# Kernel optimization log

Hardware: AMD Instinct MI355X
Metric: run time of the kernel (lower is better)

The kernel has to match this reference:

```python
import jax, jax.numpy as jnp
import numpy as np

N = 512
BATCH = 128
EPS = 1e-08


def setup_inputs() -> dict:
    key = jax.random.key(0)
    kx, kb = jax.random.split(key)
    # binary indicator of which items are present in each set
    x = jax.random.randint(kx, (BATCH, N), 0, 2, dtype=jnp.int32)
    # column-normalized random feature matrix, as in the torch __init__
    B = jax.random.normal(kb, (N, N), dtype=jnp.float32)
    B = B / jnp.linalg.norm(B, axis=0, keepdims=True)
    return {"x": x, "B": B}


def reference(x, B):
    n = B.shape[0]
    I = jnp.eye(n, dtype=B.dtype)
    L = B.T @ B + EPS * I                      # (n, n) PSD kernel
    m = (x != 0).astype(B.dtype)               # (batch, n) active-item mask
    # zero out rows and cols of inactive items, put 1 on their diagonal
    Lb = L[None, :, :] * m[:, :, None] * m[:, None, :]   # (batch, n, n)
    Lb = Lb + I[None, :, :] * (1.0 - m)[:, None, :]
    _, logdet_b = jnp.linalg.slogdet(Lb)       # (batch,)
    _, logdet_Z = jnp.linalg.slogdet(L + I)    # scalar normalizer
    return logdet_b - logdet_Z
```

## Files before the change

kernel.cpp:

```cpp
#include <hip/hip_runtime.h>
#include <math.h>

#define N 512
#define BATCH 128
#define EPS 1e-8f
#define TPB 1024
#define NW 16
#define KP 304
#define LN2 0.69314718055994530942f
#define SPLIT 160
#define GSTR 160
#define SLD2 356
#define SLAB_BYTES (352 * SLD2 * 4)

typedef _Float16 f16;
typedef _Float16 f16x8 __attribute__((ext_vector_type(8)));
typedef float f32x4 __attribute__((ext_vector_type(4)));

__device__ __forceinline__ int lh_base(int r) {
    const int a = r >> 3, b = r & 7;
    return 8 * (a + 1) * (4 * a + b);
}

#define G1_OFF   26880
#define SCR0_OFF 94848
#define M0_OFF   113280
#define SCR1_OFF 139520
#define M1_OFF   157952
#define SCR2_OFF 126720
#define M2_OFF   145152
#define ARENA_SZ 160512

__device__ __forceinline__ float rdl(float v, int l) {
    return __builtin_bit_cast(float,
        __builtin_amdgcn_readlane(__builtin_bit_cast(int, v), l));
}

__device__ __forceinline__ void tri_map(int e, int* r_out, int* c_out) {
    int rr = (int)((sqrtf(8.0f * (float)e + 1.0f) - 1.0f) * 0.5f);
    while ((((rr + 1) * (rr + 2)) >> 1) <= e) ++rr;
    while (((rr * (rr + 1)) >> 1) > e) --rr;
    *r_out = rr;
    *c_out = e - ((rr * (rr + 1)) >> 1);
}

__global__ __launch_bounds__(256) void compute_L(const float* __restrict__ B,
                                                 float* __restrict__ L) {
    const int r0 = blockIdx.x * 64, c0 = blockIdx.y * 64;
    const int tx = threadIdx.x & 15, ty = threadIdx.x >> 4;
    __shared__ float Bi[16][64];
    __shared__ float Bj[16][64];
    float acc[4][4] = {};
    for (int k0 = 0; k0 < N; k0 += 16) {
#pragma unroll
        for (int q = 0; q < 4; ++q) {
            const int e = threadIdx.x + q * 256;
            const int kr = e >> 6, cc = e & 63;
            Bi[kr][cc] = B[(k0 + kr) * N + r0 + cc];
            Bj[kr][cc] = B[(k0 + kr) * N + c0 + cc];
        }
        __syncthreads();
#pragma unroll
        for (int kq = 0; kq < 16; ++kq) {
            float a[4], b[4];
#pragma unroll
            for (int q = 0; q < 4; ++q) {
                a[q] = Bi[kq][ty * 4 + q];
                b[q] = Bj[kq][tx * 4 + q];
            }
#pragma unroll
            for (int i = 0; i < 4; ++i)
#pragma unroll
                for (int j = 0; j < 4; ++j) acc[i][j] = fmaf(a[i], b[j], acc[i][j]);
        }
        __syncthreads();
    }
#pragma unroll
    for (int i = 0; i < 4; ++i) {
        const int r = r0 + ty * 4 + i;
        f32x4 v;
#pragma unroll
        for (int j = 0; j < 4; ++j) {
            const int c = c0 + tx * 4 + j;
            v[j] = acc[i][j] + ((r == c) ? EPS : 0.0f);
        }
        *(f32x4*)(&L[r * N + c0 + tx * 4]) = v;
    }
}

template <int MODE>
__device__ __forceinline__ float gath(const float* __restrict__ L,
                                      const float* __restrict__ S, const short* idx,
                                      int k, bool add1, int gr, int gc) {
    if constexpr (MODE <= 1) {
        if (gr < k && gc < k) {
            float v = L[(int)idx[gr] * N + (int)idx[gc]];
            if (add1 && gr == gc) v += 1.0f;
            return v;
        }
        return (gr == gc) ? 1.0f : 0.0f;
    } else {
        if (gr < k && gc < k) {
            const int r2 = gr > gc ? gr : gc, c2 = gr > gc ? gc : gr;
            return S[r2 * SLD2 + c2];
        }
        return (gr == gc) ? 1.0f : 0.0f;
    }
}

template <int MODE>
__device__ float chol32(char* arena, const float* __restrict__ S,
                        const float* __restrict__ L, const short* idx,
                        int k, int rows, int ncols, bool add1) {
    const int tid = threadIdx.x;
    const int lane = tid & 63, wv = tid >> 6;
    constexpr int scr_off = (MODE == 0) ? SCR0_OFF : (MODE == 1) ? SCR1_OFF : SCR2_OFF;
    constexpr int m_off = (MODE == 0) ? M0_OFF : (MODE == 1) ? M1_OFF : M2_OFF;
    f16* Lh = (f16*)arena;
    f16* Gl = (f16*)(arena + G1_OFF);
    f16* scr = (f16*)(arena + scr_off) + wv * 576;
    f16* Mm = (f16*)(arena + m_off);
    const int frow = lane & 15, koff = (lane >> 4) * 8;
    const int crow = (lane >> 4) * 4, ccol = lane & 15;
    const f32x4 zz = {0.f, 0.f, 0.f, 0.f};

    float lg2 = 0.0f;

    auto ld_af = [&]() -> f16x8 {
        if (koff < 16) return *(const f16x8*)(&scr[frow * 36 + koff]);
        f16x8 z = {};
        return z;
    };
    auto scr_st = [&](const f32x4& v) {
#pragma unroll
        for (int q = 0; q < 4; ++q) scr[(crow + q) * 36 + ccol] = (f16)v[q];
    };
    auto factor16 = [&](int rbase, int cbase, f16* mdst) {
        float row[16], w[16];
#pragma unroll
        for (int c = 0; c < 16; ++c) row[c] = (float)scr[frow * 36 + c];
#pragma unroll
        for (int c = 0; c < 16; ++c) w[c] = (c == frow) ? 1.0f : 0.0f;
#pragma unroll
        for (int j = 0; j < 16; ++j) {
            const float piv = rdl(row[j], j);
            lg2 += __log2f(piv);
            const float irs = rsqrtf(piv);
            row[j] *= irs;
            w[j] *= irs;
#pragma unroll
            for (int cc = j + 1; cc < 16; ++cc) {
                const float s2 = rdl(row[j], cc);
                row[cc] = fmaf(-row[j], s2, row[cc]);
                w[cc] = fmaf(-s2, w[j], w[cc]);
            }
        }
        if (lane < 16) {
            f16x8 hv0, hv1;
#pragma unroll
            for (int m2 = 0; m2 < 8; ++m2) {
                hv0[m2] = (f16)row[m2];
                hv1[m2] = (f16)row[8 + m2];
            }
            *(f16x8*)(&Lh[lh_base(rbase + lane) + cbase]) = hv0;
            if (lane >= 8) *(f16x8*)(&Lh[lh_base(rbase + lane) + cbase + 8]) = hv1;
        }
        if (lane < 32) {
#pragma unroll
            for (int i = 0; i < 16; ++i)
                mdst[i * 40 + lane] = (lane < 16) ? (f16)w[i] : (f16)0.0f;
        }
    };
    auto stX = [&](const f32x4& x, int rr0, int cb) {
#pragma unroll
        for (int q = 0; q < 4; ++q) {
            const int gr = rr0 + crow + q;
            const f16 h = (f16)x[q];
            if (MODE == 1 && gr >= SPLIT) Gl[(gr - SPLIT) * GSTR + cb + ccol] = h;
            else Lh[lh_base(gr) + cb + ccol] = h;
        }
    };

    for (int jb = 0; jb < ncols; jb += 32) {
        const bool half = (ncols - jb) <= 16;
        const int nkk = jb >> 5;
        const int ntile = (rows - jb) >> 4;
        const int nbelow = ntile - (half ? 1 : 2);
        const int rb0 = jb + (half ? 16 : 32);

        bool val_[2] = {false, false};
        int r0_[2] = {0, 0};
        f16x8 afs_[2] = {};
        f32x4 s1_[2] = {};

        if (wv == 0) {
            f32x4 g00 = zz, g10 = zz, g11 = zz;
#pragma unroll
            for (int q = 0; q < 4; ++q)
                g00[q] = gath<MODE>(L, S, idx, k, add1, jb + crow + q, jb + ccol);
            if (!half) {
#pragma unroll
                for (int q = 0; q < 4; ++q) {
                    g10[q] = gath<MODE>(L, S, idx, k, add1, jb + 16 + crow + q, jb + ccol);
                    g11[q] = gath<MODE>(L, S, idx, k, add1, jb + 16 + crow + q, jb + 16 + ccol);
                }
            }
            const int bF0 = lh_base(jb + frow) + koff;
            const int bF1 = lh_base(jb + 16 + frow) + koff;
            f32x4 a00 = zz, a10 = zz, a11 = zz;
            for (int c = 0; c < nkk; ++c) {
                const int kk = c << 5;
                const f16x8 F0 = *(const f16x8*)(&Lh[bF0 + kk]);
                a00 = __builtin_amdgcn_mfma_f32_16x16x32_f16(F0, F0, a00, 0, 0, 0);
                if (!half) {
                    const f16x8 F1 = *(const f16x8*)(&Lh[bF1 + kk]);
                    a10 = __builtin_amdgcn_mfma_f32_16x16x32_f16(F1, F0, a10, 0, 0, 0);
                    a11 = __builtin_amdgcn_mfma_f32_16x16x32_f16(F1, F1, a11, 0, 0, 0);
                }
            }
            f32x4 s00;
#pragma unroll
            for (int q = 0; q < 4; ++q) s00[q] = g00[q] - a00[q];
            scr_st(s00);
            factor16(jb, jb, Mm);
            if (!half) {
                f32x4 s10;
#pragma unroll
                for (int q = 0; q < 4; ++q) s10[q] = g10[q] - a10[q];
                scr_st(s10);
                const f16x8 af10 = ld_af();
                const f16x8 bM0 = *(const f16x8*)(&Mm[frow * 40 + koff]);
                const f32x4 x10 = __builtin_amdgcn_mfma_f32_16x16x32_f16(af10, bM0, zz, 0, 0, 0);
#pragma unroll
                for (int q = 0; q < 4; ++q)
                    Lh[lh_base(jb + 16 + crow + q) + jb + ccol] = (f16)x10[q];
                scr_st(x10);
                const f16x8 afx = ld_af();
                const f32x4 pr = __builtin_amdgcn_mfma_f32_16x16x32_f16(afx, afx, zz, 0, 0, 0);
                f32x4 s11;
#pragma unroll
                for (int q = 0; q < 4; ++q) s11[q] = g11[q] - a11[q] - pr[q];
                scr_st(s11);
                factor16(jb + 16, jb + 16, Mm + 640);
            }
        } else {
            bool isg_[2];
            int baseA_[2];
#pragma unroll
            for (int it = 0; it < 2; ++it) {
                const int tb = (wv - 1) + 15 * it;
                val_[it] = tb < nbelow;
                const int rr = rb0 + 16 * (val_[it] ? tb : 0);
                r0_[it] = rr;
                isg_[it] = (MODE == 1) && val_[it] && (rr >= SPLIT);
                baseA_[it] = isg_[it] ? ((rr - SPLIT + frow) * GSTR + koff)
                                      : (lh_base(rr + frow) + koff);
            }
            f32x4 g0_[2] = {zz, zz}, g1_[2] = {zz, zz};
#pragma unroll
            for (int it = 0; it < 2; ++it)
                if (val_[it]) {
#pragma unroll
                    for (int q = 0; q < 4; ++q) {
                        g0_[it][q] = gath<MODE>(L, S, idx, k, add1, r0_[it] + crow + q, jb + ccol);
                        if (!half)
                            g1_[it][q] = gath<MODE>(L, S, idx, k, add1, r0_[it] + crow + q, jb + 16 + ccol);
                    }
                }
            const int bB0 = lh_base(jb + frow) + koff;
            const int bB1 = lh_base(jb + 16 + frow) + koff;
            f32x4 ac0_[2] = {zz, zz}, ac1_[2] = {zz, zz};
            for (int c = 0; c < nkk; ++c) {
                const int kk = c << 5;
                const f16x8 B0 = *(const f16x8*)(&Lh[bB0 + kk]);
                f16x8 B1 = {};
                if (!half) B1 = *(const f16x8*)(&Lh[bB1 + kk]);
#pragma unroll
                for (int it = 0; it < 2; ++it)
                    if (val_[it]) {
                        const f16x8 A = isg_[it] ? *(const f16x8*)(&Gl[baseA_[it] + kk])
                                                 : *(const f16x8*)(&Lh[baseA_[it] + kk]);
                        ac0_[it] = __builtin_amdgcn_mfma_f32_16x16x32_f16(A, B0, ac0_[it], 0, 0, 0);
                        if (!half)
                            ac1_[it] = __builtin_amdgcn_mfma_f32_16x16x32_f16(A, B1, ac1_[it], 0, 0, 0);
                    }
            }
#pragma unroll
            for (int it = 0; it < 2; ++it)
                if (val_[it]) {
                    f32x4 s0;
#pragma unroll
                    for (int q = 0; q < 4; ++q) s0[q] = g0_[it][q] - ac0_[it][q];
                    scr_st(s0);
                    afs_[it] = ld_af();
                    if (!half) {
#pragma unroll
                        for (int q = 0; q < 4; ++q) s1_[it][q] = g1_[it][q] - ac1_[it][q];
                    }
                }
        }
        __syncthreads();

        {
            const f16x8 bM0 = *(const f16x8*)(&Mm[frow * 40 + koff]);
            f16x8 bM1 = {}, bX10 = {};
            if (!half) {
                bM1 = *(const f16x8*)(&Mm[640 + frow * 40 + koff]);
                bX10 = *(const f16x8*)(&Lh[lh_base(jb + 16 + frow) + jb + koff]);
            }
#pragma unroll
            for (int it = 0; it < 2; ++it)
                if (val_[it]) {
                    const f32x4 x0 = __builtin_amdgcn_mfma_f32_16x16x32_f16(afs_[it], bM0, zz, 0, 0, 0);
                    stX(x0, r0_[it], jb);
                    if (!half) {
                        scr_st(x0);
                        const f16x8 afx = ld_af();
                        const f32x4 pr = __builtin_amdgcn_mfma_f32_16x16x32_f16(afx, bX10, zz, 0, 0, 0);
                        f32x4 s1p;
#pragma unroll
                        for (int q = 0; q < 4; ++q) s1p[q] = s1_[it][q] - pr[q];
                        scr_st(s1p);
                        const f16x8 af1 = ld_af();
                        const f32x4 x1 = __builtin_amdgcn_mfma_f32_16x16x32_f16(af1, bM1, zz, 0, 0, 0);
                        stX(x1, r0_[it], jb + 16);
                    }
                }
        }
        __syncthreads();
    }
    return lg2;
}

__device__ void schur32(char* arena, float* __restrict__ S,
                        const float* __restrict__ L, const short* idx,
                        int k, int k2p, bool add1) {
    const int tid = threadIdx.x;
    const int lane = tid & 63, wv = tid >> 6;
    const f16* Gl = (const f16*)(arena + G1_OFF);
    const int frow = lane & 15, koff = (lane >> 4) * 8;
    const int crow = (lane >> 4) * 4, ccol = lane & 15;
    const int nt2 = k2p >> 4, TT = (nt2 * (nt2 + 1)) >> 1;
    for (int e = wv; e < TT; e += NW) {
        int R, C;
        tri_map(e, &R, &C);
        const int r0 = R << 4, c0 = C << 4;
        f32x4 g;
#pragma unroll
        for (int q = 0; q < 4; ++q) {
            const int gr = SPLIT + r0 + crow + q, gc = SPLIT + c0 + ccol;
            float v;
            if (gr < k && gc < k) {
                v = L[(int)idx[gr] * N + (int)idx[gc]];
                if (add1 && gr == gc) v += 1.0f;
            } else v = (gr == gc) ? 1.0f : 0.0f;
            g[q] = v;
        }
        const int ba = (r0 + frow) * GSTR + koff, bb = (c0 + frow) * GSTR + koff;
        f32x4 acc = {0.f, 0.f, 0.f, 0.f};
#pragma unroll
        for (int c = 0; c < SPLIT / 32; ++c) {
            const f16x8 A = *(const f16x8*)(&Gl[ba + (c << 5)]);
            const f16x8 B = *(const f16x8*)(&Gl[bb + (c << 5)]);
            acc = __builtin_amdgcn_mfma_f32_16x16x32_f16(A, B, acc, 0, 0, 0);
        }
#pragma unroll
        for (int q = 0; q < 4; ++q)
            S[(r0 + crow + q) * SLD2 + c0 + ccol] = g[q] - acc[q];
    }
}

__global__ __launch_bounds__(TPB, 4) void chol_all(const int* __restrict__ x,
                                                   const float* __restrict__ L,
                                                   char* __restrict__ slabs, int nslabs,
                                                   float* __restrict__ logs) {
    const int b = blockIdx.x;
    const int tid = threadIdx.x;
    const int lane = tid & 63, wv = tid >> 6;
    __shared__ __align__(16) char arena[ARENA_SZ];
    __shared__ short idx[N];
    __shared__ int wcnt[NW];

    const bool zc = (b == BATCH);
    const bool inx = tid < N;
    const bool act = zc ? inx : (inx && x[(size_t)b * N + tid] != 0);
    const unsigned long long m = __ballot(act);
    if (lane == 0) wcnt[wv] = __popcll(m);
    __syncthreads();
    int off = 0, ktot = 0;
    for (int q = 0; q < NW; ++q) {
        if (q < wv) off += wcnt[q];
        ktot += wcnt[q];
    }
    if (act) idx[off + __popcll(m & ((1ULL << lane) - 1ULL))] = (short)tid;
    __syncthreads();

    const int k = ktot;
    const int kp = (k + 15) & ~15;

    float lg2;
    if (!zc && kp <= KP) {
        lg2 = chol32<0>(arena, nullptr, L, idx, k, kp, kp, false);
    } else {
        const int si = zc ? 0 : (nslabs > 1 ? 1 + (b % (nslabs - 1)) : 0);
        float* S = (float*)(slabs + (size_t)si * SLAB_BYTES);
        const int k2 = k - SPLIT, k2p = kp - SPLIT;
        lg2 = chol32<1>(arena, nullptr, L, idx, k, kp, SPLIT, zc);
        schur32(arena, S, L, idx, k, k2p, zc);
        __syncthreads();
        lg2 += chol32<2>(arena, S, L, idx, k2, k2p, k2p, false);
    }
    if (tid == 0) logs[b] = lg2 * LN2;
}

__global__ void finalize(const float* __restrict__ logs, float* __restrict__ out) {
    const int i = threadIdx.x;
    out[i] = logs[i] - logs[BATCH];
}

extern "C" void kernel_launch(void* const* d_in, const int* in_sizes, int n_in,
                              void* d_out, int out_size, void* d_ws, size_t ws_size,
                              hipStream_t stream) {
    const int* x = (const int*)d_in[0];
    const float* B = (const float*)d_in[1];
    float* out = (float*)d_out;

    char* ws = (char*)d_ws;
    const size_t L_bytes = (size_t)N * N * 4;
    float* L = (float*)ws;
    float* logs = (float*)(ws + L_bytes);
    const size_t head = L_bytes + 4096;
    char* slabs = ws + head;
    int nslabs = (ws_size > head) ? (int)((ws_size - head) / SLAB_BYTES) : 1;
    if (nslabs < 1) nslabs = 1;
    if (nslabs > 9) nslabs = 9;

    compute_L<<<dim3(8, 8), 256, 0, stream>>>(B, L);
    chol_all<<<BATCH + 1, TPB, 0, stream>>>(x, L, slabs, nslabs, logs);
    finalize<<<1, BATCH, 0, stream>>>(logs, out);
}
```

Before: 160.9 us.

## Factor 32x32 diagonal blocks in one pass and solve panels via explicit inverse

Restructures the blocked Cholesky so wave 0 factors the whole 32x32 diagonal block in registers and writes its inverse to LDS. The other waves then solve both 16-column halves of each panel tile with two MFMAs against that inverse. This replaces the old chain of two 16x16 factorizations with an intermediate product and second solve. Padding is now to multiples of 32, the small-path cutoff is raised to 320, and the k-loops load four chunks before issuing MFMAs to hide LDS latency. In exchange, wave 0 runs a longer serial 32-step elimination, padding to 32 can add wasted rows, and inverting a 32x32 block in fp16 may cost accuracy.

New measurement: 274.8 us. 1.71x slower.

```diff
diff --git a/kernel.cpp b/kernel.cpp
--- a/kernel.cpp
+++ b/kernel.cpp
@@ -6,7 +6,7 @@
 #define EPS 1e-8f
 #define TPB 1024
 #define NW 16
-#define KP 304
+#define KP 320
 #define LN2 0.69314718055994530942f
 #define SPLIT 160
 #define GSTR 160
@@ -23,13 +23,9 @@
 }
 
 #define G1_OFF   26880
-#define SCR0_OFF 94848
-#define M0_OFF   113280
-#define SCR1_OFF 139520
-#define M1_OFF   157952
-#define SCR2_OFF 126720
-#define M2_OFF   145152
-#define ARENA_SZ 160512
+#define DW_OFF   139520
+#define SCR_OFF  142080
+#define ARENA_SZ 161280
 
 __device__ __forceinline__ float rdl(float v, int l) {
     return __builtin_bit_cast(float,
@@ -109,139 +105,102 @@
 }
 
 template <int MODE>
-__device__ float chol32(char* arena, const float* __restrict__ S,
-                        const float* __restrict__ L, const short* idx,
-                        int k, int rows, int ncols, bool add1) {
+__device__ float cholp(char* arena, const float* __restrict__ S,
+                       const float* __restrict__ L, const short* idx,
+                       int k, int rows, int ncols, bool add1) {
     const int tid = threadIdx.x;
     const int lane = tid & 63, wv = tid >> 6;
-    constexpr int scr_off = (MODE == 0) ? SCR0_OFF : (MODE == 1) ? SCR1_OFF : SCR2_OFF;
-    constexpr int m_off = (MODE == 0) ? M0_OFF : (MODE == 1) ? M1_OFF : M2_OFF;
     f16* Lh = (f16*)arena;
     f16* Gl = (f16*)(arena + G1_OFF);
-    f16* scr = (f16*)(arena + scr_off) + wv * 576;
-    f16* Mm = (f16*)(arena + m_off);
+    f16* DW = (f16*)(arena + DW_OFF);
+    f16* scrw = (f16*)(arena + SCR_OFF) + (wv > 0 ? (wv - 1) * 640 : 0);
     const int frow = lane & 15, koff = (lane >> 4) * 8;
     const int crow = (lane >> 4) * 4, ccol = lane & 15;
     const f32x4 zz = {0.f, 0.f, 0.f, 0.f};
 
     float lg2 = 0.0f;
-
-    auto ld_af = [&]() -> f16x8 {
-        if (koff < 16) return *(const f16x8*)(&scr[frow * 36 + koff]);
-        f16x8 z = {};
-        return z;
-    };
-    auto scr_st = [&](const f32x4& v) {
-#pragma unroll
-        for (int q = 0; q < 4; ++q) scr[(crow + q) * 36 + ccol] = (f16)v[q];
-    };
-    auto factor16 = [&](int rbase, int cbase, f16* mdst) {
-        float row[16], w[16];
-#pragma unroll
-        for (int c = 0; c < 16; ++c) row[c] = (float)scr[frow * 36 + c];
-#pragma unroll
-        for (int c = 0; c < 16; ++c) w[c] = (c == frow) ? 1.0f : 0.0f;
-#pragma unroll
-        for (int j = 0; j < 16; ++j) {
-            const float piv = rdl(row[j], j);
-            lg2 += __log2f(piv);
-            const float irs = rsqrtf(piv);
-            row[j] *= irs;
-            w[j] *= irs;
-#pragma unroll
-            for (int cc = j + 1; cc < 16; ++cc) {
-                const float s2 = rdl(row[j], cc);
-                row[cc] = fmaf(-row[j], s2, row[cc]);
-                w[cc] = fmaf(-s2, w[j], w[cc]);
-            }
-        }
-        if (lane < 16) {
-            f16x8 hv0, hv1;
-#pragma unroll
-            for (int m2 = 0; m2 < 8; ++m2) {
-                hv0[m2] = (f16)row[m2];
-                hv1[m2] = (f16)row[8 + m2];
-            }
-            *(f16x8*)(&Lh[lh_base(rbase + lane) + cbase]) = hv0;
-            if (lane >= 8) *(f16x8*)(&Lh[lh_base(rbase + lane) + cbase + 8]) = hv1;
-        }
-        if (lane < 32) {
-#pragma unroll
-            for (int i = 0; i < 16; ++i)
-                mdst[i * 40 + lane] = (lane < 16) ? (f16)w[i] : (f16)0.0f;
-        }
-    };
-    auto stX = [&](const f32x4& x, int rr0, int cb) {
-#pragma unroll
-        for (int q = 0; q < 4; ++q) {
-            const int gr = rr0 + crow + q;
-            const f16 h = (f16)x[q];
-            if (MODE == 1 && gr >= SPLIT) Gl[(gr - SPLIT) * GSTR + cb + ccol] = h;
-            else Lh[lh_base(gr) + cb + ccol] = h;
-        }
-    };
-
     for (int jb = 0; jb < ncols; jb += 32) {
-        const bool half = (ncols - jb) <= 16;
         const int nkk = jb >> 5;
-        const int ntile = (rows - jb) >> 4;
-        const int nbelow = ntile - (half ? 1 : 2);
-        const int rb0 = jb + (half ? 16 : 32);
+        const int nbelow = (rows - jb - 32) >> 4;
 
         bool val_[2] = {false, false};
         int r0_[2] = {0, 0};
         f16x8 afs_[2] = {};
-        f32x4 s1_[2] = {};
 
         if (wv == 0) {
             f32x4 g00 = zz, g10 = zz, g11 = zz;
 #pragma unroll
-            for (int q = 0; q < 4; ++q)
+            for (int q = 0; q < 4; ++q) {
                 g00[q] = gath<MODE>(L, S, idx, k, add1, jb + crow + q, jb + ccol);
-            if (!half) {
-#pragma unroll
-                for (int q = 0; q < 4; ++q) {
-                    g10[q] = gath<MODE>(L, S, idx, k, add1, jb + 16 + crow + q, jb + ccol);
-                    g11[q] = gath<MODE>(L, S, idx, k, add1, jb + 16 + crow + q, jb + 16 + ccol);
-                }
+                g10[q] = gath<MODE>(L, S, idx, k, add1, jb + 16 + crow + q, jb + ccol);
+                g11[q] = gath<MODE>(L, S, idx, k, add1, jb + 16 + crow + q, jb + 16 + ccol);
             }
             const int bF0 = lh_base(jb + frow) + koff;
             const int bF1 = lh_base(jb + 16 + frow) + koff;
             f32x4 a00 = zz, a10 = zz, a11 = zz;
-            for (int c = 0; c < nkk; ++c) {
-                const int kk = c << 5;
-                const f16x8 F0 = *(const f16x8*)(&Lh[bF0 + kk]);
-                a00 = __builtin_amdgcn_mfma_f32_16x16x32_f16(F0, F0, a00, 0, 0, 0);
-                if (!half) {
-                    const f16x8 F1 = *(const f16x8*)(&Lh[bF1 + kk]);
-                    a10 = __builtin_amdgcn_mfma_f32_16x16x32_f16(F1, F0, a10, 0, 0, 0);
-                    a11 = __builtin_amdgcn_mfma_f32_16x16x32_f16(F1, F1, a11, 0, 0, 0);
-                }
-            }
-            f32x4 s00;
-#pragma unroll
-            for (int q = 0; q < 4; ++q) s00[q] = g00[q] - a00[q];
-            scr_st(s00);
-            factor16(jb, jb, Mm);
-            if (!half) {
-                f32x4 s10;
-#pragma unroll
-                for (int q = 0; q < 4; ++q) s10[q] = g10[q] - a10[q];
-                scr_st(s10);
-                const f16x8 af10 = ld_af();
-                const f16x8 bM0 = *(const f16x8*)(&Mm[frow * 40 + koff]);
-                const f32x4 x10 = __builtin_amdgcn_mfma_f32_16x16x32_f16(af10, bM0, zz, 0, 0, 0);
-#pragma unroll
-                for (int q = 0; q < 4; ++q)
-                    Lh[lh_base(jb + 16 + crow + q) + jb + ccol] = (f16)x10[q];
-                scr_st(x10);
-                const f16x8 afx = ld_af();
-                const f32x4 pr = __builtin_amdgcn_mfma_f32_16x16x32_f16(afx, afx, zz, 0, 0, 0);
-                f32x4 s11;
-#pragma unroll
-                for (int q = 0; q < 4; ++q) s11[q] = g11[q] - a11[q] - pr[q];
-                scr_st(s11);
-                factor16(jb + 16, jb + 16, Mm + 640);
+            for (int cg = 0; cg < nkk; cg += 4) {
+                f16x8 F0_[4], F1_[4];
+#pragma unroll
+                for (int u = 0; u < 4; ++u) {
+                    const int c = cg + u;
+                    const bool ok = c < nkk;
+                    F0_[u] = ok ? *(const f16x8*)(&Lh[bF0 + (c << 5)]) : (f16x8){};
+                    F1_[u] = ok ? *(const f16x8*)(&Lh[bF1 + (c << 5)]) : (f16x8){};
+                }
+#pragma unroll
+                for (int u = 0; u < 4; ++u)
+                    if (cg + u < nkk) {
+                        a00 = __builtin_amdgcn_mfma_f32_16x16x32_f16(F0_[u], F0_[u], a00, 0, 0, 0);
+                        a10 = __builtin_amdgcn_mfma_f32_16x16x32_f16(F1_[u], F0_[u], a10, 0, 0, 0);
+                        a11 = __builtin_amdgcn_mfma_f32_16x16x32_f16(F1_[u], F1_[u], a11, 0, 0, 0);
+                    }
+            }
+#pragma unroll
+            for (int q = 0; q < 4; ++q) {
+                DW[(crow + q) * 40 + ccol] = (f16)(g00[q] - a00[q]);
+                DW[(16 + crow + q) * 40 + ccol] = (f16)(g10[q] - a10[q]);
+                DW[(16 + crow + q) * 40 + 16 + ccol] = (f16)(g11[q] - a11[q]);
+            }
+            const int r = lane & 31;
+            float row[32], w[32];
+#pragma unroll
+            for (int m = 0; m < 4; ++m) {
+                const f16x8 hv = *(const f16x8*)(&DW[r * 40 + 8 * m]);
+#pragma unroll
+                for (int e = 0; e < 8; ++e) row[8 * m + e] = (float)hv[e];
+            }
+#pragma unroll
+            for (int c = 0; c < 32; ++c) w[c] = (c == r) ? 1.0f : 0.0f;
+#pragma unroll
+            for (int j = 0; j < 32; ++j) {
+                const float piv = rdl(row[j], j);
+                lg2 += __log2f(piv);
+                const float irs = rsqrtf(piv);
+                row[j] *= irs;
+                w[j] *= irs;
+#pragma unroll
+                for (int cc = j + 1; cc < 32; ++cc) {
+                    const float s2 = rdl(row[j], cc);
+                    row[cc] = fmaf(-row[j], s2, row[cc]);
+                    w[cc] = fmaf(-s2, w[j], w[cc]);
+                }
+            }
+            if (lane < 32) {
+                const int nch = (lane >> 3) + 1;
+#pragma unroll
+                for (int m = 0; m < 4; ++m) {
+                    if (m < nch) {
+                        f16x8 hv;
+#pragma unroll
+                        for (int e = 0; e < 8; ++e) {
+                            const int c = 8 * m + e;
+                            hv[e] = (f16)((c > lane) ? 0.0f : row[c]);
+                        }
+                        *(f16x8*)(&Lh[lh_base(jb + lane) + jb + 8 * m]) = hv;
+                    }
+                }
+#pragma unroll
+                for (int i = 0; i < 32; ++i) DW[i * 40 + lane] = (f16)w[i];
             }
         } else {
             bool isg_[2];
@@ -250,7 +209,7 @@
             for (int it = 0; it < 2; ++it) {
                 const int tb = (wv - 1) + 15 * it;
                 val_[it] = tb < nbelow;
-                const int rr = rb0 + 16 * (val_[it] ? tb : 0);
+                const int rr = jb + 32 + 16 * (val_[it] ? tb : 0);
                 r0_[it] = rr;
                 isg_[it] = (MODE == 1) && val_[it] && (rr >= SPLIT);
                 baseA_[it] = isg_[it] ? ((rr - SPLIT + frow) * GSTR + koff)
@@ -263,67 +222,75 @@
 #pragma unroll
                     for (int q = 0; q < 4; ++q) {
                         g0_[it][q] = gath<MODE>(L, S, idx, k, add1, r0_[it] + crow + q, jb + ccol);
-                        if (!half)
-                            g1_[it][q] = gath<MODE>(L, S, idx, k, add1, r0_[it] + crow + q, jb + 16 + ccol);
+                        g1_[it][q] = gath<MODE>(L, S, idx, k, add1, r0_[it] + crow + q, jb + 16 + ccol);
                     }
                 }
             const int bB0 = lh_base(jb + frow) + koff;
             const int bB1 = lh_base(jb + 16 + frow) + koff;
             f32x4 ac0_[2] = {zz, zz}, ac1_[2] = {zz, zz};
-            for (int c = 0; c < nkk; ++c) {
-                const int kk = c << 5;
-                const f16x8 B0 = *(const f16x8*)(&Lh[bB0 + kk]);
-                f16x8 B1 = {};
-                if (!half) B1 = *(const f16x8*)(&Lh[bB1 + kk]);
-#pragma unroll
-                for (int it = 0; it < 2; ++it)
-                    if (val_[it]) {
-                        const f16x8 A = isg_[it] ? *(const f16x8*)(&Gl[baseA_[it] + kk])
-                                                 : *(const f16x8*)(&Lh[baseA_[it] + kk]);
-                        ac0_[it] = __builtin_amdgcn_mfma_f32_16x16x32_f16(A, B0, ac0_[it], 0, 0, 0);
-                        if (!half)
-                            ac1_[it] = __builtin_amdgcn_mfma_f32_16x16x32_f16(A, B1, ac1_[it], 0, 0, 0);
+            for (int cg = 0; cg < nkk; cg += 4) {
+                f16x8 B0_[4], B1_[4], A_[4][2];
+#pragma unroll
+                for (int u = 0; u < 4; ++u) {
+                    const int c = cg + u;
+                    const bool ok = c < nkk;
+                    const int kk = c << 5;
+                    B0_[u] = ok ? *(const f16x8*)(&Lh[bB0 + kk]) : (f16x8){};
+                    B1_[u] = ok ? *(const f16x8*)(&Lh[bB1 + kk]) : (f16x8){};
+#pragma unroll
+                    for (int it = 0; it < 2; ++it) {
+                        f16x8 vv = {};
+                        if (ok && val_[it])
+                            vv = isg_[it] ? *(const f16x8*)(&Gl[baseA_[it] + kk])
+                                          : *(const f16x8*)(&Lh[baseA_[it] + kk]);
+                        A_[u][it] = vv;
+                    }
+                }
+#pragma unroll
+                for (int u = 0; u < 4; ++u)
+                    if (cg + u < nkk) {
+#pragma unroll
+                        for (int it = 0; it < 2; ++it)
+                            if (val_[it]) {
+                                ac0_[it] = __builtin_amdgcn_mfma_f32_16x16x32_f16(
+                                    A_[u][it], B0_[u], ac0_[it], 0, 0, 0);
+                                ac1_[it] = __builtin_amdgcn_mfma_f32_16x16x32_f16(
+                                    A_[u][it], B1_[u], ac1_[it], 0, 0, 0);
+                            }
                     }
             }
 #pragma unroll
             for (int it = 0; it < 2; ++it)
                 if (val_[it]) {
-                    f32x4 s0;
-#pragma unroll
-                    for (int q = 0; q < 4; ++q) s0[q] = g0_[it][q] - ac0_[it][q];
-                    scr_st(s0);
-                    afs_[it] = ld_af();
-                    if (!half) {
-#pragma unroll
-                        for (int q = 0; q < 4; ++q) s1_[it][q] = g1_[it][q] - ac1_[it][q];
-                    }
+#pragma unroll
+                    for (int q = 0; q < 4; ++q) {
+                        scrw[(crow + q) * 40 + ccol] = (f16)(g0_[it][q] - ac0_[it][q]);
+                        scrw[(crow + q) * 40 + 16 + ccol] = (f16)(g1_[it][q] - ac1_[it][q]);
+                    }
+                    afs_[it] = *(const f16x8*)(&scrw[frow * 40 + koff]);
                 }
         }
         __syncthreads();
 
         {
-            const f16x8 bM0 = *(const f16x8*)(&Mm[frow * 40 + koff]);
-            f16x8 bM1 = {}, bX10 = {};
-            if (!half) {
-                bM1 = *(const f16x8*)(&Mm[640 + frow * 40 + koff]);
-                bX10 = *(const f16x8*)(&Lh[lh_base(jb + 16 + frow) + jb + koff]);
-            }
+            const f16x8 bW0 = *(const f16x8*)(&DW[frow * 40 + koff]);
+            const f16x8 bW1 = *(const f16x8*)(&DW[(16 + frow) * 40 + koff]);
 #pragma unroll
             for (int it = 0; it < 2; ++it)
                 if (val_[it]) {
-                    const f32x4 x0 = __builtin_amdgcn_mfma_f32_16x16x32_f16(afs_[it], bM0, zz, 0, 0, 0);
-                    stX(x0, r0_[it], jb);
-                    if (!half) {
-                        scr_st(x0);
-                        const f16x8 afx = ld_af();
-                        const f32x4 pr = __builtin_amdgcn_mfma_f32_16x16x32_f16(afx, bX10, zz, 0, 0, 0);
-                        f32x4 s1p;
-#pragma unroll
-                        for (int q = 0; q < 4; ++q) s1p[q] = s1_[it][q] - pr[q];
-                        scr_st(s1p);
-                        const f16x8 af1 = ld_af();
-                        const f32x4 x1 = __builtin_amdgcn_mfma_f32_16x16x32_f16(af1, bM1, zz, 0, 0, 0);
-                        stX(x1, r0_[it], jb + 16);
+                    const f32x4 x0 = __builtin_amdgcn_mfma_f32_16x16x32_f16(afs_[it], bW0, zz, 0, 0, 0);
+                    const f32x4 x1 = __builtin_amdgcn_mfma_f32_16x16x32_f16(afs_[it], bW1, zz, 0, 0, 0);
+#pragma unroll
+                    for (int q = 0; q < 4; ++q) {
+                        const int gr = r0_[it] + crow + q;
+                        const f16 h0 = (f16)x0[q], h1 = (f16)x1[q];
+                        if (MODE == 1 && gr >= SPLIT) {
+                            Gl[(gr - SPLIT) * GSTR + jb + ccol] = h0;
+                            Gl[(gr - SPLIT) * GSTR + jb + 16 + ccol] = h1;
+                        } else {
+                            Lh[lh_base(gr) + jb + ccol] = h0;
+                            Lh[lh_base(gr) + jb + 16 + ccol] = h1;
+                        }
                     }
                 }
         }
@@ -396,19 +363,19 @@
     __syncthreads();
 
     const int k = ktot;
-    const int kp = (k + 15) & ~15;
+    const int kp = (k + 31) & ~31;
 
     float lg2;
     if (!zc && kp <= KP) {
-        lg2 = chol32<0>(arena, nullptr, L, idx, k, kp, kp, false);
+        lg2 = cholp<0>(arena, nullptr, L, idx, k, kp, kp, false);
     } else {
         const int si = zc ? 0 : (nslabs > 1 ? 1 + (b % (nslabs - 1)) : 0);
         float* S = (float*)(slabs + (size_t)si * SLAB_BYTES);
         const int k2 = k - SPLIT, k2p = kp - SPLIT;
-        lg2 = chol32<1>(arena, nullptr, L, idx, k, kp, SPLIT, zc);
+        lg2 = cholp<1>(arena, nullptr, L, idx, k, kp, SPLIT, zc);
         schur32(arena, S, L, idx, k, k2p, zc);
         __syncthreads();
-        lg2 += chol32<2>(arena, S, L, idx, k2, k2p, k2p, false);
+        lg2 += cholp<2>(arena, S, L, idx, k2, k2p, k2p, false);
     }
     if (tid == 0) logs[b] = lg2 * LN2;
 }
```
